# Optimization experiments

Measured on AMD Instinct MI355X. Metric: run time of the kernel, lower is better.

## Reference

```python
import jax, jax.numpy as jnp
import numpy as np
import math

D_PAIR = 64
N_HEADS = 4
D_HEAD = D_PAIR // N_HEADS


def setup_inputs() -> dict:
    key = jax.random.key(0)
    ks = jax.random.split(key, 9)
    B, L, D = 2, 256, D_PAIR
    s = 1.0 / math.sqrt(D)
    return {
        "z": jax.random.normal(ks[0], (B, L, L, D), dtype=jnp.float32),
        "ln_scale": jnp.ones((D,), jnp.float32),
        "ln_bias": jnp.zeros((D,), jnp.float32),
        "Wq": jax.random.normal(ks[1], (D, D), jnp.float32) * s,
        "Wk": jax.random.normal(ks[2], (D, D), jnp.float32) * s,
        "Wv": jax.random.normal(ks[3], (D, D), jnp.float32) * s,
        "Wg": jax.random.normal(ks[4], (D, D), jnp.float32) * s,
        "bg": jax.random.normal(ks[5], (D,), jnp.float32) * 0.02,
        "Wo": jax.random.normal(ks[6], (D, D), jnp.float32) * s,
        "bo": jax.random.normal(ks[7], (D,), jnp.float32) * 0.02,
    }


def _layernorm(x, scale, bias, eps=1e-5):
    mu = jnp.mean(x, axis=-1, keepdims=True)
    var = jnp.var(x, axis=-1, keepdims=True)
    return (x - mu) * jax.lax.rsqrt(var + eps) * scale + bias


def reference(z, ln_scale, ln_bias, Wq, Wk, Wv, Wg, bg, Wo, bo):
    B, L, _, D = z.shape
    H, Dh = N_HEADS, D_HEAD
    zn = _layernorm(z, ln_scale, ln_bias)
    # torch Linear(no bias): x @ W.T
    Q = (zn @ Wq.T).reshape(B, L, L, H, Dh)
    K = (zn @ Wk.T).reshape(B, L, L, H, Dh)
    V = (zn @ Wv.T).reshape(B, L, L, H, Dh)
    scale = 1.0 / math.sqrt(Dh)
    # row-wise attention: for each row l, attend over column index j
    attn = jnp.einsum("blihd,bljhd->blhij", Q, K) * scale  # [B,L,H,L,L]
    attn = jax.nn.softmax(attn, axis=-1)
    out = jnp.einsum("blhij,bljhd->blihd", attn, V).reshape(B, L, L, D)
    gate = jax.nn.sigmoid(zn @ Wg.T + bg)
    out = gate * out
    return out @ Wo.T + bo
```

## Files before the change

### kernel.cpp

```cpp
#include <hip/hip_runtime.h>
#include <hip/hip_bf16.h>
#include <math.h>


typedef __attribute__((ext_vector_type(4))) float f32x4;
typedef __attribute__((ext_vector_type(8))) short s16x8;
typedef __attribute__((ext_vector_type(4))) short s16x4;

#define MFMA16(a, b, c) __builtin_amdgcn_mfma_f32_16x16x32_bf16((a), (b), (c), 0, 0, 0)

__device__ __forceinline__ f32x4 mfma16b(s16x4 a, s16x4 b, f32x4 c) {
#if __has_builtin(__builtin_amdgcn_mfma_f32_16x16x16bf16_1k)
    return __builtin_amdgcn_mfma_f32_16x16x16bf16_1k(a, b, c, 0, 0, 0);
#elif __has_builtin(__builtin_amdgcn_mfma_f32_16x16x16_bf16)
    return __builtin_amdgcn_mfma_f32_16x16x16_bf16(a, b, c, 0, 0, 0);
#else
    f32x4 d;
    asm volatile("s_nop 1\n\t"
                 "v_mfma_f32_16x16x16_bf16 %0, %1, %2, %3\n\t"
                 "s_nop 7\n\t"
                 "s_nop 7"
                 : "=v"(d) : "v"(a), "v"(b), "v"(c));
    return d;
#endif
}

__device__ __forceinline__ float exp2a(float x) {
    float r;
    asm("v_exp_f32 %0, %1" : "=v"(r) : "v"(x));
    return r;
}
__device__ __forceinline__ float rcpa(float x) {
    float r;
    asm("v_rcp_f32 %0, %1" : "=v"(r) : "v"(x));
    return r;
}

__device__ __forceinline__ unsigned pk2(float a, float b) {
    union { __hip_bfloat162 h; unsigned u; } c;
    float2 t; t.x = a; t.y = b;
    c.h = __float22bfloat162_rn(t);
    return c.u;
}
__device__ __forceinline__ s16x8 cvt8(const float* p) {
    union { unsigned u[4]; s16x8 v; } r;
    r.u[0] = pk2(p[0], p[1]); r.u[1] = pk2(p[2], p[3]);
    r.u[2] = pk2(p[4], p[5]); r.u[3] = pk2(p[6], p[7]);
    return r.v;
}

__global__ __launch_bounds__(256, 2)
void k0_ln(const float* __restrict__ z, const float* __restrict__ ln_s,
           const float* __restrict__ ln_b, short* __restrict__ znG)
{
    const size_t row = (size_t)blockIdx.x * 256 + threadIdx.x;
    float zn[64];
    const float4* zp4 = (const float4*)(z + row * 64);
    #pragma unroll
    for (int gq = 0; gq < 16; ++gq) {
        float4 v4 = zp4[gq];
        zn[gq * 4 + 0] = v4.x; zn[gq * 4 + 1] = v4.y;
        zn[gq * 4 + 2] = v4.z; zn[gq * 4 + 3] = v4.w;
    }
    float mu = 0.f;
    #pragma unroll
    for (int k = 0; k < 64; ++k) mu += zn[k];
    mu *= (1.f / 64.f);
    float va = 0.f;
    #pragma unroll
    for (int k = 0; k < 64; ++k) { float d = zn[k] - mu; va += d * d; }
    const float rs = rsqrtf(va * (1.f / 64.f) + 1e-5f);
    #pragma unroll
    for (int k = 0; k < 64; ++k) zn[k] = (zn[k] - mu) * rs * ln_s[k] + ln_b[k];
    union { unsigned u[32]; uint4 q[8]; } pk;
    #pragma unroll
    for (int k = 0; k < 32; ++k) pk.u[k] = pk2(zn[2 * k], zn[2 * k + 1]);
    uint4* dst = (uint4*)(znG + row * 64);
    #pragma unroll
    for (int i = 0; i < 8; ++i) dst[i] = pk.q[i];
}

static constexpr int KSH = 0;
static constexpr int VT  = 5120;
static constexpr int LDS_EL = 9344;

__global__ __launch_bounds__(256, 3)
void ka_fused(const short* __restrict__ znG, const float* __restrict__ Wq,
              const float* __restrict__ Wk, const float* __restrict__ Wv,
              const float* __restrict__ Wg, const float* __restrict__ bg,
              short* __restrict__ ws)
{
    __shared__ __align__(16) short lds[LDS_EL];
    const int tid = threadIdx.x, lane = tid & 63, w = tid >> 6;
    const int n16 = lane & 15, quad = lane >> 4;
    const int g = blockIdx.x, bl = g & 511, h = g >> 9;
    const int wsl_rows = w * 64;

    s16x8 bq[2], bk[2], bv[2], bgf[2];
    #pragma unroll
    for (int ks = 0; ks < 2; ++ks) {
        size_t off = (size_t)(h * 16 + n16) * 64 + ks * 32 + quad * 8;
        bq[ks] = cvt8(Wq + off);  bk[ks] = cvt8(Wk + off);
        bv[ks] = cvt8(Wv + off);  bgf[ks] = cvt8(Wg + off);
    }
    const float4 bg4 = *(const float4*)(bg + h * 16 + quad * 4);
    constexpr float QS  = 0.25f;
    constexpr float L2E = 1.44269504088896340736f;

    float g4t[4][4];
    s16x4 qa4[4];
    #pragma unroll
    for (int t = 0; t < 4; ++t) {
        const short* zr = znG + ((size_t)bl * 256 + wsl_rows + t * 16 + n16) * 64
                          + quad * 8;
        s16x8 zn0 = *(const s16x8*)zr;
        s16x8 zn1 = *(const s16x8*)(zr + 32);
        f32x4 aq = {}, ak = {}, av = {}, ag = {};
        aq = MFMA16(bq[0], zn0, aq);  aq = MFMA16(bq[1], zn1, aq);
        ak = MFMA16(bk[0], zn0, ak);  ak = MFMA16(bk[1], zn1, ak);
        ag = MFMA16(bgf[0], zn0, ag); ag = MFMA16(bgf[1], zn1, ag);
        av = MFMA16(zn0, bv[0], av);  av = MFMA16(zn1, bv[1], av);
        {
            union { unsigned u[2]; s16x4 v; } q;
            q.u[0] = pk2(aq[0] * QS, aq[1] * QS);
            q.u[1] = pk2(aq[2] * QS, aq[3] * QS);
            qa4[t] = q.v;
        }
        {
            uint2 p = {pk2(ak[0], ak[1]), pk2(ak[2], ak[3])};
            *(uint2*)&lds[KSH + (wsl_rows + t * 16 + n16) * 20 + quad * 4] = p;
        }
        {
            uint2 p = {pk2(av[0], av[1]), pk2(av[2], av[3])};
            *(uint2*)&lds[VT + n16 * 264 + (wsl_rows + t * 16 + quad * 4)] = p;
        }
        #pragma unroll
        for (int r = 0; r < 4; ++r) {
            float x = ag[r] + bg4[r];
            g4t[t][r] = rcpa(1.f + exp2a(x * -L2E));
        }
    }
    __syncthreads();

    f32x4 o4[4], lacc[4];
    #pragma unroll
    for (int qt = 0; qt < 4; ++qt) { o4[qt] = {}; lacc[qt] = {}; }
    s16x4 ones4;
    {
        union { unsigned u[2]; s16x4 v; } c;
        c.u[0] = 0x3F803F80u; c.u[1] = 0x3F803F80u;
        ones4 = c.v;
    }
    const int kbase = KSH + n16 * 20 + quad * 4;
    const int vbase = VT + n16 * 264 + quad * 4;
    for (int ch = 0; ch < 8; ++ch) {
        #pragma unroll
        for (int jtl = 0; jtl < 2; ++jtl) {
            const int jt = ch * 2 + jtl;
            s16x4 kf = *(const s16x4*)&lds[kbase + jt * 320];
            s16x4 vf = *(const s16x4*)&lds[vbase + jt * 16];
            #pragma unroll
            for (int qt = 0; qt < 4; ++qt) {
                f32x4 zc = {};
                f32x4 s = mfma16b(kf, qa4[qt], zc);
                float e0 = exp2a(s[0] * L2E), e1 = exp2a(s[1] * L2E);
                float e2 = exp2a(s[2] * L2E), e3 = exp2a(s[3] * L2E);
                union { unsigned u[2]; s16x4 v; } pb;
                pb.u[0] = pk2(e0, e1); pb.u[1] = pk2(e2, e3);
                o4[qt]   = mfma16b(vf, pb.v, o4[qt]);
                lacc[qt] = mfma16b(ones4, pb.v, lacc[qt]);
            }
        }
    }

    #pragma unroll
    for (int qt = 0; qt < 4; ++qt) {
        const float l = (lacc[qt][0] + lacc[qt][1]) * 0.5f;
        const float inv = rcpa(l);
        float g0 = g4t[qt][0] * o4[qt][0] * inv;
        float g1 = g4t[qt][1] * o4[qt][1] * inv;
        float g2 = g4t[qt][2] * o4[qt][2] * inv;
        float g3 = g4t[qt][3] * o4[qt][3] * inv;
        uint2 p = {pk2(g0, g1), pk2(g2, g3)};
        short* dst = ws + (((size_t)h * 512 + bl) * 256 + wsl_rows + qt * 16 + n16) * 16
                     + quad * 4;
        *(uint2*)dst = p;
    }
}

__global__ __launch_bounds__(256, 2)
void k3_out(const short* __restrict__ ws, const float* __restrict__ Wo,
            const float* __restrict__ bo, float* __restrict__ out)
{
    const int tid = threadIdx.x, lane = tid & 63, w = tid >> 6;
    const int n16 = lane & 15, quad = lane >> 4;
    const short* GO = ws;
    const int bl = blockIdx.x & 511, half = blockIdx.x >> 9;
    const int rowloc = half * 128 + w * 32;

    s16x8 bfr[4][2];
    #pragma unroll
    for (int nt = 0; nt < 4; ++nt)
        #pragma unroll
        for (int ks = 0; ks < 2; ++ks)
            bfr[nt][ks] = cvt8(Wo + (size_t)(nt * 16 + n16) * 64 + ks * 32 + quad * 8);

    f32x4 acc[2][4] = {};
    #pragma unroll
    for (int mt = 0; mt < 2; ++mt) {
        #pragma unroll
        for (int c = 0; c < 2; ++c) {
            int hp = c * 2 + (quad >> 1);
            const short* ap = &GO[(((size_t)hp * 512 + bl) * 256 + rowloc + mt * 16 + n16) * 16
                                  + (quad & 1) * 8];
            s16x8 a = *(const s16x8*)ap;
            #pragma unroll
            for (int nt = 0; nt < 4; ++nt)
                acc[mt][nt] = MFMA16(bfr[nt][c], a, acc[mt][nt]);
        }
    }
    #pragma unroll
    for (int nt = 0; nt < 4; ++nt) {
        const float4 b4 = *(const float4*)(bo + nt * 16 + quad * 4);
        f32x4 b4v; b4v[0] = b4.x; b4v[1] = b4.y; b4v[2] = b4.z; b4v[3] = b4.w;
        #pragma unroll
        for (int mt = 0; mt < 2; ++mt) {
            f32x4 v = acc[mt][nt] + b4v;
            *(f32x4*)&out[((size_t)bl * 256 + rowloc + mt * 16 + n16) * 64
                          + nt * 16 + quad * 4] = v;
        }
    }
}

extern "C" void kernel_launch(void* const* d_in, const int* in_sizes, int n_in,
                              void* d_out, int out_size, void* d_ws, size_t ws_size,
                              hipStream_t stream) {
    const float* z  = (const float*)d_in[0];
    const float* ls = (const float*)d_in[1];
    const float* lb = (const float*)d_in[2];
    const float* Wq = (const float*)d_in[3];
    const float* Wk = (const float*)d_in[4];
    const float* Wv = (const float*)d_in[5];
    const float* Wg = (const float*)d_in[6];
    const float* bg = (const float*)d_in[7];
    const float* Wo = (const float*)d_in[8];
    const float* bo = (const float*)d_in[9];
    float* out = (float*)d_out;
    short* wsp = (short*)d_ws;
    short* znG = (short*)d_out;

    hipLaunchKernelGGL(k0_ln, dim3(512), dim3(256), 0, stream, z, ls, lb, znG);
    hipLaunchKernelGGL(ka_fused, dim3(2048), dim3(256), 0, stream,
                       znG, Wq, Wk, Wv, Wg, bg, wsp);
    hipLaunchKernelGGL(k3_out, dim3(1024), dim3(256), 0, stream, wsp, Wo, bo, out);
}
```

Before: 157.0 us.

## Fuse layernorm, per-head attention and output projection into one kernel

Replaces three launches (layernorm, per-head attention, output projection) with a single kernel. Each block handles one row l, keeps the bf16 normalized row in swizzled LDS, and loops over the four heads. Each head's gated attention output feeds the Wo projection through MFMA accumulated in registers. This removes the global round trips of the normalized activations and the per-head workspace plus two launch overheads. In exchange the grid drops from 2048 to 512 blocks, the head loop runs serially within a block, and register and LDS pressure rise, which may reduce occupancy and parallelism.

```diff
diff --git a/kernel.cpp b/kernel.cpp
--- a/kernel.cpp
+++ b/kernel.cpp
@@ -48,185 +48,180 @@
     r.u[2] = pk2(p[4], p[5]); r.u[3] = pk2(p[6], p[7]);
     return r.v;
 }
+__device__ __forceinline__ s16x4 cvt4(const float* p) {
+    union { unsigned u[2]; s16x4 v; } r;
+    r.u[0] = pk2(p[0], p[1]); r.u[1] = pk2(p[2], p[3]);
+    return r.v;
+}
+
+static constexpr int ZNL = 0;
+static constexpr int KSH = 16384;
+static constexpr int VT  = 21504;
+static constexpr int LDS_EL = 25728;
 
 __global__ __launch_bounds__(256, 2)
-void k0_ln(const float* __restrict__ z, const float* __restrict__ ln_s,
-           const float* __restrict__ ln_b, short* __restrict__ znG)
-{
-    const size_t row = (size_t)blockIdx.x * 256 + threadIdx.x;
-    float zn[64];
-    const float4* zp4 = (const float4*)(z + row * 64);
-    #pragma unroll
-    for (int gq = 0; gq < 16; ++gq) {
-        float4 v4 = zp4[gq];
-        zn[gq * 4 + 0] = v4.x; zn[gq * 4 + 1] = v4.y;
-        zn[gq * 4 + 2] = v4.z; zn[gq * 4 + 3] = v4.w;
-    }
-    float mu = 0.f;
-    #pragma unroll
-    for (int k = 0; k < 64; ++k) mu += zn[k];
-    mu *= (1.f / 64.f);
-    float va = 0.f;
-    #pragma unroll
-    for (int k = 0; k < 64; ++k) { float d = zn[k] - mu; va += d * d; }
-    const float rs = rsqrtf(va * (1.f / 64.f) + 1e-5f);
-    #pragma unroll
-    for (int k = 0; k < 64; ++k) zn[k] = (zn[k] - mu) * rs * ln_s[k] + ln_b[k];
-    union { unsigned u[32]; uint4 q[8]; } pk;
-    #pragma unroll
-    for (int k = 0; k < 32; ++k) pk.u[k] = pk2(zn[2 * k], zn[2 * k + 1]);
-    uint4* dst = (uint4*)(znG + row * 64);
-    #pragma unroll
-    for (int i = 0; i < 8; ++i) dst[i] = pk.q[i];
-}
-
-static constexpr int KSH = 0;
-static constexpr int VT  = 5120;
-static constexpr int LDS_EL = 9344;
-
-__global__ __launch_bounds__(256, 3)
-void ka_fused(const short* __restrict__ znG, const float* __restrict__ Wq,
-              const float* __restrict__ Wk, const float* __restrict__ Wv,
-              const float* __restrict__ Wg, const float* __restrict__ bg,
-              short* __restrict__ ws)
+void ka_all(const float* __restrict__ z, const float* __restrict__ ln_s,
+            const float* __restrict__ ln_b, const float* __restrict__ Wq,
+            const float* __restrict__ Wk, const float* __restrict__ Wv,
+            const float* __restrict__ Wg, const float* __restrict__ bg,
+            const float* __restrict__ Wo, const float* __restrict__ bo,
+            float* __restrict__ out)
 {
     __shared__ __align__(16) short lds[LDS_EL];
     const int tid = threadIdx.x, lane = tid & 63, w = tid >> 6;
     const int n16 = lane & 15, quad = lane >> 4;
-    const int g = blockIdx.x, bl = g & 511, h = g >> 9;
-    const int wsl_rows = w * 64;
-
-    s16x8 bq[2], bk[2], bv[2], bgf[2];
-    #pragma unroll
-    for (int ks = 0; ks < 2; ++ks) {
-        size_t off = (size_t)(h * 16 + n16) * 64 + ks * 32 + quad * 8;
-        bq[ks] = cvt8(Wq + off);  bk[ks] = cvt8(Wk + off);
-        bv[ks] = cvt8(Wv + off);  bgf[ks] = cvt8(Wg + off);
-    }
-    const float4 bg4 = *(const float4*)(bg + h * 16 + quad * 4);
+    const int bl = blockIdx.x;
+    const int wsl = w * 4096;
+    const int wrows = w * 64;
+
+    {
+        float zn[64];
+        const float4* zp4 = (const float4*)(z + ((size_t)bl * 256 + tid) * 64);
+        #pragma unroll
+        for (int gq = 0; gq < 16; ++gq) {
+            float4 v4 = zp4[gq];
+            zn[gq * 4 + 0] = v4.x; zn[gq * 4 + 1] = v4.y;
+            zn[gq * 4 + 2] = v4.z; zn[gq * 4 + 3] = v4.w;
+        }
+        float mu = 0.f;
+        #pragma unroll
+        for (int k = 0; k < 64; ++k) mu += zn[k];
+        mu *= (1.f / 64.f);
+        float va = 0.f;
+        #pragma unroll
+        for (int k = 0; k < 64; ++k) { float d = zn[k] - mu; va += d * d; }
+        const float rs = rsqrtf(va * (1.f / 64.f) + 1e-5f);
+        #pragma unroll
+        for (int k = 0; k < 64; ++k) zn[k] = (zn[k] - mu) * rs * ln_s[k] + ln_b[k];
+        const int lr = lane;
+        #pragma unroll
+        for (int gq = 0; gq < 8; ++gq) {
+            union { unsigned u[4]; s16x8 v; } pkv;
+            pkv.u[0] = pk2(zn[gq * 8 + 0], zn[gq * 8 + 1]);
+            pkv.u[1] = pk2(zn[gq * 8 + 2], zn[gq * 8 + 3]);
+            pkv.u[2] = pk2(zn[gq * 8 + 4], zn[gq * 8 + 5]);
+            pkv.u[3] = pk2(zn[gq * 8 + 6], zn[gq * 8 + 7]);
+            *(s16x8*)&lds[ZNL + wsl + (lr >> 4) * 1024 + (lr & 15) * 64
+                          + ((gq ^ (lr & 7)) * 8)] = pkv.v;
+        }
+    }
+
     constexpr float QS  = 0.25f;
     constexpr float L2E = 1.44269504088896340736f;
-
-    float g4t[4][4];
-    s16x4 qa4[4];
-    #pragma unroll
-    for (int t = 0; t < 4; ++t) {
-        const short* zr = znG + ((size_t)bl * 256 + wsl_rows + t * 16 + n16) * 64
-                          + quad * 8;
-        s16x8 zn0 = *(const s16x8*)zr;
-        s16x8 zn1 = *(const s16x8*)(zr + 32);
-        f32x4 aq = {}, ak = {}, av = {}, ag = {};
-        aq = MFMA16(bq[0], zn0, aq);  aq = MFMA16(bq[1], zn1, aq);
-        ak = MFMA16(bk[0], zn0, ak);  ak = MFMA16(bk[1], zn1, ak);
-        ag = MFMA16(bgf[0], zn0, ag); ag = MFMA16(bgf[1], zn1, ag);
-        av = MFMA16(zn0, bv[0], av);  av = MFMA16(zn1, bv[1], av);
-        {
-            union { unsigned u[2]; s16x4 v; } q;
-            q.u[0] = pk2(aq[0] * QS, aq[1] * QS);
-            q.u[1] = pk2(aq[2] * QS, aq[3] * QS);
-            qa4[t] = q.v;
-        }
-        {
-            uint2 p = {pk2(ak[0], ak[1]), pk2(ak[2], ak[3])};
-            *(uint2*)&lds[KSH + (wsl_rows + t * 16 + n16) * 20 + quad * 4] = p;
-        }
-        {
-            uint2 p = {pk2(av[0], av[1]), pk2(av[2], av[3])};
-            *(uint2*)&lds[VT + n16 * 264 + (wsl_rows + t * 16 + quad * 4)] = p;
-        }
-        #pragma unroll
-        for (int r = 0; r < 4; ++r) {
-            float x = ag[r] + bg4[r];
-            g4t[t][r] = rcpa(1.f + exp2a(x * -L2E));
-        }
-    }
-    __syncthreads();
-
-    f32x4 o4[4], lacc[4];
-    #pragma unroll
-    for (int qt = 0; qt < 4; ++qt) { o4[qt] = {}; lacc[qt] = {}; }
     s16x4 ones4;
     {
         union { unsigned u[2]; s16x4 v; } c;
         c.u[0] = 0x3F803F80u; c.u[1] = 0x3F803F80u;
         ones4 = c.v;
     }
-    const int kbase = KSH + n16 * 20 + quad * 4;
-    const int vbase = VT + n16 * 264 + quad * 4;
-    for (int ch = 0; ch < 8; ++ch) {
-        #pragma unroll
-        for (int jtl = 0; jtl < 2; ++jtl) {
-            const int jt = ch * 2 + jtl;
-            s16x4 kf = *(const s16x4*)&lds[kbase + jt * 320];
-            s16x4 vf = *(const s16x4*)&lds[vbase + jt * 16];
+
+    f32x4 acc_out[4][4];
+    #pragma unroll
+    for (int qt = 0; qt < 4; ++qt)
+        #pragma unroll
+        for (int nt = 0; nt < 4; ++nt) acc_out[qt][nt] = {};
+
+    for (int h = 0; h < 4; ++h) {
+        s16x8 bq[2], bk[2], bv[2], bgf[2];
+        #pragma unroll
+        for (int ks = 0; ks < 2; ++ks) {
+            size_t off = (size_t)(h * 16 + n16) * 64 + ks * 32 + quad * 8;
+            bq[ks] = cvt8(Wq + off);  bk[ks] = cvt8(Wk + off);
+            bv[ks] = cvt8(Wv + off);  bgf[ks] = cvt8(Wg + off);
+        }
+        const float4 bg4 = *(const float4*)(bg + h * 16 + quad * 4);
+
+        float g4t[4][4];
+        s16x4 qa4[4];
+        #pragma unroll
+        for (int t = 0; t < 4; ++t) {
+            s16x8 zn0 = *(const s16x8*)&lds[ZNL + wsl + t * 1024 + n16 * 64
+                                            + ((quad ^ (n16 & 7)) * 8)];
+            s16x8 zn1 = *(const s16x8*)&lds[ZNL + wsl + t * 1024 + n16 * 64
+                                            + (((4 + quad) ^ (n16 & 7)) * 8)];
+            f32x4 aq = {}, ak = {}, av = {}, ag = {};
+            aq = MFMA16(bq[0], zn0, aq);  aq = MFMA16(bq[1], zn1, aq);
+            ak = MFMA16(bk[0], zn0, ak);  ak = MFMA16(bk[1], zn1, ak);
+            ag = MFMA16(bgf[0], zn0, ag); ag = MFMA16(bgf[1], zn1, ag);
+            av = MFMA16(zn0, bv[0], av);  av = MFMA16(zn1, bv[1], av);
+            {
+                union { unsigned u[2]; s16x4 v; } q;
+                q.u[0] = pk2(aq[0] * QS, aq[1] * QS);
+                q.u[1] = pk2(aq[2] * QS, aq[3] * QS);
+                qa4[t] = q.v;
+            }
+            {
+                uint2 p = {pk2(ak[0], ak[1]), pk2(ak[2], ak[3])};
+                *(uint2*)&lds[KSH + (wrows + t * 16 + n16) * 20 + quad * 4] = p;
+            }
+            {
+                uint2 p = {pk2(av[0], av[1]), pk2(av[2], av[3])};
+                *(uint2*)&lds[VT + n16 * 264 + (wrows + t * 16 + quad * 4)] = p;
+            }
             #pragma unroll
-            for (int qt = 0; qt < 4; ++qt) {
-                f32x4 zc = {};
-                f32x4 s = mfma16b(kf, qa4[qt], zc);
-                float e0 = exp2a(s[0] * L2E), e1 = exp2a(s[1] * L2E);
-                float e2 = exp2a(s[2] * L2E), e3 = exp2a(s[3] * L2E);
-                union { unsigned u[2]; s16x4 v; } pb;
-                pb.u[0] = pk2(e0, e1); pb.u[1] = pk2(e2, e3);
-                o4[qt]   = mfma16b(vf, pb.v, o4[qt]);
-                lacc[qt] = mfma16b(ones4, pb.v, lacc[qt]);
-            }
-        }
-    }
-
-    #pragma unroll
-    for (int qt = 0; qt < 4; ++qt) {
-        const float l = (lacc[qt][0] + lacc[qt][1]) * 0.5f;
-        const float inv = rcpa(l);
-        float g0 = g4t[qt][0] * o4[qt][0] * inv;
-        float g1 = g4t[qt][1] * o4[qt][1] * inv;
-        float g2 = g4t[qt][2] * o4[qt][2] * inv;
-        float g3 = g4t[qt][3] * o4[qt][3] * inv;
-        uint2 p = {pk2(g0, g1), pk2(g2, g3)};
-        short* dst = ws + (((size_t)h * 512 + bl) * 256 + wsl_rows + qt * 16 + n16) * 16
-                     + quad * 4;
-        *(uint2*)dst = p;
-    }
-}
-
-__global__ __launch_bounds__(256, 2)
-void k3_out(const short* __restrict__ ws, const float* __restrict__ Wo,
-            const float* __restrict__ bo, float* __restrict__ out)
-{
-    const int tid = threadIdx.x, lane = tid & 63, w = tid >> 6;
-    const int n16 = lane & 15, quad = lane >> 4;
-    const short* GO = ws;
-    const int bl = blockIdx.x & 511, half = blockIdx.x >> 9;
-    const int rowloc = half * 128 + w * 32;
-
-    s16x8 bfr[4][2];
-    #pragma unroll
-    for (int nt = 0; nt < 4; ++nt)
-        #pragma unroll
-        for (int ks = 0; ks < 2; ++ks)
-            bfr[nt][ks] = cvt8(Wo + (size_t)(nt * 16 + n16) * 64 + ks * 32 + quad * 8);
-
-    f32x4 acc[2][4] = {};
-    #pragma unroll
-    for (int mt = 0; mt < 2; ++mt) {
-        #pragma unroll
-        for (int c = 0; c < 2; ++c) {
-            int hp = c * 2 + (quad >> 1);
-            const short* ap = &GO[(((size_t)hp * 512 + bl) * 256 + rowloc + mt * 16 + n16) * 16
-                                  + (quad & 1) * 8];
-            s16x8 a = *(const s16x8*)ap;
+            for (int r = 0; r < 4; ++r) {
+                float x = ag[r] + bg4[r];
+                g4t[t][r] = rcpa(1.f + exp2a(x * -L2E));
+            }
+        }
+        __syncthreads();
+
+        f32x4 o4[4], lacc[4];
+        #pragma unroll
+        for (int qt = 0; qt < 4; ++qt) { o4[qt] = {}; lacc[qt] = {}; }
+        const int kbase = KSH + n16 * 20 + quad * 4;
+        const int vbase = VT + n16 * 264 + quad * 4;
+        for (int ch = 0; ch < 8; ++ch) {
             #pragma unroll
-            for (int nt = 0; nt < 4; ++nt)
-                acc[mt][nt] = MFMA16(bfr[nt][c], a, acc[mt][nt]);
-        }
-    }
+            for (int jtl = 0; jtl < 2; ++jtl) {
+                const int jt = ch * 2 + jtl;
+                s16x4 kf = *(const s16x4*)&lds[kbase + jt * 320];
+                s16x4 vf = *(const s16x4*)&lds[vbase + jt * 16];
+                #pragma unroll
+                for (int qt = 0; qt < 4; ++qt) {
+                    f32x4 zc = {};
+                    f32x4 s = mfma16b(kf, qa4[qt], zc);
+                    float e0 = exp2a(s[0] * L2E), e1 = exp2a(s[1] * L2E);
+                    float e2 = exp2a(s[2] * L2E), e3 = exp2a(s[3] * L2E);
+                    union { unsigned u[2]; s16x4 v; } pb;
+                    pb.u[0] = pk2(e0, e1); pb.u[1] = pk2(e2, e3);
+                    o4[qt]   = mfma16b(vf, pb.v, o4[qt]);
+                    lacc[qt] = mfma16b(ones4, pb.v, lacc[qt]);
+                }
+            }
+        }
+
+        s16x4 goB[4];
+        #pragma unroll
+        for (int qt = 0; qt < 4; ++qt) {
+            const float l = (lacc[qt][0] + lacc[qt][1]) * 0.5f;
+            const float inv = rcpa(l);
+            float g0 = g4t[qt][0] * o4[qt][0] * inv;
+            float g1 = g4t[qt][1] * o4[qt][1] * inv;
+            float g2 = g4t[qt][2] * o4[qt][2] * inv;
+            float g3 = g4t[qt][3] * o4[qt][3] * inv;
+            union { unsigned u[2]; s16x4 v; } pb;
+            pb.u[0] = pk2(g0, g1); pb.u[1] = pk2(g2, g3);
+            goB[qt] = pb.v;
+        }
+        #pragma unroll
+        for (int nt = 0; nt < 4; ++nt) {
+            s16x4 wof = cvt4(Wo + (size_t)(nt * 16 + n16) * 64 + h * 16 + quad * 4);
+            #pragma unroll
+            for (int qt = 0; qt < 4; ++qt)
+                acc_out[qt][nt] = mfma16b(wof, goB[qt], acc_out[qt][nt]);
+        }
+        __syncthreads();
+    }
+
     #pragma unroll
     for (int nt = 0; nt < 4; ++nt) {
         const float4 b4 = *(const float4*)(bo + nt * 16 + quad * 4);
         f32x4 b4v; b4v[0] = b4.x; b4v[1] = b4.y; b4v[2] = b4.z; b4v[3] = b4.w;
         #pragma unroll
-        for (int mt = 0; mt < 2; ++mt) {
-            f32x4 v = acc[mt][nt] + b4v;
-            *(f32x4*)&out[((size_t)bl * 256 + rowloc + mt * 16 + n16) * 64
+        for (int qt = 0; qt < 4; ++qt) {
+            f32x4 v = acc_out[qt][nt] + b4v;
+            *(f32x4*)&out[((size_t)bl * 256 + wrows + qt * 16 + n16) * 64
                           + nt * 16 + quad * 4] = v;
         }
     }
@@ -246,11 +241,7 @@
     const float* Wo = (const float*)d_in[8];
     const float* bo = (const float*)d_in[9];
     float* out = (float*)d_out;
-    short* wsp = (short*)d_ws;
-    short* znG = (short*)d_out;
-
-    hipLaunchKernelGGL(k0_ln, dim3(512), dim3(256), 0, stream, z, ls, lb, znG);
-    hipLaunchKernelGGL(ka_fused, dim3(2048), dim3(256), 0, stream,
-                       znG, Wq, Wk, Wv, Wg, bg, wsp);
-    hipLaunchKernelGGL(k3_out, dim3(1024), dim3(256), 0, stream, wsp, Wo, bo, out);
-}
+
+    hipLaunchKernelGGL(ka_all, dim3(512), dim3(256), 0, stream,
+                       z, ls, lb, Wq, Wk, Wv, Wg, bg, Wo, bo, out);
+}
```

Result: faster. 143.8 us (-8.4%).
